# Kernel tuning notes

Measured on AMD Instinct MI355X. Metric: run time of the kernel, lower is better.

## Reference

```python
import jax, jax.numpy as jnp
import numpy as np
from jax import lax

NUM_STEPS = 100
T_FINAL = 1.0
BATCH = 16384
DIM = 64


def make_G(key, d, beta=1.0):
    # new_G: each G[:, :, k] is skew-symmetric, then globally rescaled so that
    # trace(L_G) == -0.5 * d, with L_G = 0.5 * einsum('ijk,jmk->im', G, G).
    F = jax.random.normal(key, (d, d, d), dtype=jnp.float32)  # F[:, :, k]
    G = 0.5 * (F - jnp.swapaxes(F, 0, 1))
    L_G = 0.5 * jnp.einsum('ijk,jmk->im', G, G)
    tr_L = jnp.trace(L_G)
    G = jnp.sqrt(-0.5 * d / tr_L) * G
    return jnp.sqrt(beta) * G


def setup_inputs() -> dict:
    key = jax.random.key(0)
    k_y0, k_t, k_G, k_dW = jax.random.split(key, 4)
    y0 = jax.random.normal(k_y0, (BATCH, DIM), dtype=jnp.float32)
    t = jax.random.uniform(k_t, (BATCH,), dtype=jnp.float32) * T_FINAL  # times in [0, T)
    G = make_G(k_G, DIM, beta=1.0)
    dt = T_FINAL / NUM_STEPS
    # Brownian increments for each RK4 step, dW ~ N(0, dt I)
    dW = jax.random.normal(k_dW, (NUM_STEPS, BATCH, DIM), dtype=jnp.float32) * np.sqrt(dt).astype(np.float32)
    return {"y0": y0, "t": t, "G": G, "dW": dW}


def reference(y0, t, G, dW):
    # multiplicativeNoise.sample -> sample_scheme: 100-step RK4 Stratonovich
    # integration of dY = mu_Strato dt + G(Y) o dB, then per-sample time gather.
    n = NUM_STEPS
    dt = T_FINAL / n
    L_G = 0.5 * jnp.einsum('ijk,jmk->im', G, G)  # [d, d]

    def mu_strato(y):
        # f(t,y) - 0.5 * div_Sigma(t,y) = L_G y - L_G y (kept explicit for faithfulness)
        f = jnp.einsum('ij,bj->bi', L_G, y)
        div_sigma = jnp.einsum('ij,bj->bi', 2.0 * L_G, y)
        return f - 0.5 * div_sigma

    def increment(y, dw):
        # drift * dt + (G y) . dW ; fuse the [b, d, d] diffusion contraction
        return mu_strato(y) * dt + jnp.einsum('ijk,bj,bk->bi', G, y, dw)

    def rk4_step(y, dw):
        k1 = increment(y, dw)
        k2 = increment(y + 0.5 * k1, dw)
        k3 = increment(y + 0.5 * k2, dw)
        k4 = increment(y + k3, dw)
        y_new = y + (k1 + 2.0 * k2 + 2.0 * k3 + k4) / 6.0
        return y_new, y_new

    _, ys = lax.scan(rk4_step, y0, dW)  # [n, b, d]

    # num_steps_int = trunc(n * t / T), clamped to n-1 when t >= T
    idx = jnp.clip(jnp.trunc(n * t / T_FINAL).astype(jnp.int32), 0, n - 1)  # [b]
    yt = ys[idx, jnp.arange(y0.shape[0])]  # [b, d]
    return yt
```

## Files before the change

### kernel.cpp

```cpp
#include <hip/hip_runtime.h>


typedef __attribute__((ext_vector_type(8))) short short8;
typedef __attribute__((ext_vector_type(4))) float f32x4;

#define NSTEP 100
#define BATCH 16384
#define NCHUNK 1024
#define ISTR 72
#define ESTR 4616

__device__ __forceinline__ unsigned short f2bf(float f) {
  unsigned u = __float_as_uint(f);
  unsigned r = (u + 0x7FFFu + ((u >> 16) & 1u)) >> 16;
  return (unsigned short)r;
}
__device__ __forceinline__ unsigned pack2(float a, float b) {
  return (unsigned)f2bf(a) | ((unsigned)f2bf(b) << 16);
}
__device__ __forceinline__ float bflo(unsigned u) { return __uint_as_float(u << 16); }
__device__ __forceinline__ float bfhi(unsigned u) { return __uint_as_float(u & 0xffff0000u); }


__global__ void k_swz(const float* __restrict__ G, unsigned short* __restrict__ g2s) {
  int o = blockIdx.x * blockDim.x + threadIdx.x;
  if (o < 64 * 64 * 64) {
    int nt = o >> 10;
    int r  = o & 1023;
    int l  = r >> 4;
    int c  = (r >> 3) & 1;
    int j  = r & 7;
    int n  = (nt << 4) + (l & 15);
    int k  = (c << 5) + ((l >> 4) << 3) + j;
    g2s[o] = f2bf(G[(n << 6) + k]);
  }
}

__global__ void k_idx(const float* __restrict__ t, int* __restrict__ idxb, int* __restrict__ hist) {
  int b = blockIdx.x * blockDim.x + threadIdx.x;
  if (b < BATCH) {
    int ix = (int)truncf(100.0f * t[b]);
    ix = min(max(ix, 0), NSTEP - 1);
    idxb[b] = ix;
    atomicAdd(&hist[ix], 1);
  }
}

__global__ void k_scan(const int* __restrict__ hist, int* __restrict__ offs) {
  if (threadIdx.x == 0 && blockIdx.x == 0) {
    int run = 0;
    for (int i = 0; i < NSTEP; ++i) { offs[i] = run; run += hist[i]; }
  }
}

__global__ void k_scatter(const int* __restrict__ idxb, const int* __restrict__ offs,
                          int* __restrict__ cur, int* __restrict__ perm) {
  int b = blockIdx.x * blockDim.x + threadIdx.x;
  if (b < BATCH) {
    int ix = idxb[b];
    int pos = offs[ix] + atomicAdd(&cur[ix], 1);
    perm[pos] = b;
  }
}


__device__ __forceinline__ float rk4_dot(const unsigned* Ap, const float* vr) {
  float a0 = 0.f, a1 = 0.f, a2 = 0.f, a3 = 0.f;
#pragma unroll
  for (int m = 0; m < 16; ++m) {
    float4 v = ((const float4*)vr)[m];
    unsigned ua = Ap[2 * m], ub = Ap[2 * m + 1];
    a0 = fmaf(bflo(ua), v.x, a0);
    a1 = fmaf(bfhi(ua), v.y, a1);
    a2 = fmaf(bflo(ub), v.z, a2);
    a3 = fmaf(bfhi(ub), v.w, a3);
  }
  return (a0 + a1) + (a2 + a3);
}

__device__ __forceinline__ float rk4_one(const unsigned short* Ar, float* vr, float y, int lane) {
  unsigned Areg[32];
#pragma unroll
  for (int m = 0; m < 8; ++m) {
    uint4 q = *(const uint4*)(Ar + (m << 3));
    Areg[4 * m + 0] = q.x; Areg[4 * m + 1] = q.y;
    Areg[4 * m + 2] = q.z; Areg[4 * m + 3] = q.w;
  }
  float k1 = rk4_dot(Areg, vr);
  vr[lane] = fmaf(0.5f, k1, y);
  float k2 = rk4_dot(Areg, vr);
  vr[lane] = fmaf(0.5f, k2, y);
  float k3 = rk4_dot(Areg, vr);
  vr[lane] = y + k3;
  float k4 = rk4_dot(Areg, vr);
  float yn = y + (k1 + 2.f * k2 + 2.f * k3 + k4) * (1.f / 6.f);
  vr[lane] = yn;
  return yn;
}

__global__ void __launch_bounds__(1024, 1) k_main(
    const float* __restrict__ y0, const float* __restrict__ dW,
    const unsigned short* __restrict__ G2S, const int* __restrict__ perm,
    const int* __restrict__ idxb, float* __restrict__ out)
{
  __shared__ __align__(16) unsigned short Abuf[16 * ESTR];
  __shared__ __align__(16) unsigned short dwst[1024];
  __shared__ __align__(16) float vbuf[16 * 64];
  __shared__ int meta_b[16], meta_i[16], chunk_max;

  const int t = threadIdx.x;
  const int lane = t & 63;
  const int wave = t >> 6;

  int W = blockIdx.x;
  int c = (W & 1) ? (NCHUNK - 1 - (W >> 1)) : (W >> 1);

  if (t < 16) {
    int b = perm[(c << 4) + t];
    meta_b[t] = b;
    meta_i[t] = idxb[b];
  }
  __syncthreads();
  if (t == 0) {
    int m = 0;
    for (int e = 0; e < 16; ++e) m = max(m, meta_i[e]);
    chunk_max = m;
  }
  const int my_b = meta_b[wave];
  const int my_idx = meta_i[wave];
  float y = y0[my_b * 64 + lane];
  vbuf[(wave << 6) + lane] = y;
  __syncthreads();
  const int nsteps = chunk_max + 1;

  const int fl = lane & 15;
  const int fq = lane >> 4;
  const int di = ((lane >> 3) << 7) + (wave << 3) + (lane & 7);
  float* vr = &vbuf[wave << 6];

  float dv = dW[(0 * BATCH + my_b) * 64 + lane];

  for (int s = 0; s < nsteps; ++s) {
    dwst[di] = f2bf(dv);
    if (s + 1 < nsteps) dv = dW[((s + 1) * BATCH + my_b) * 64 + lane];
    __syncthreads();

    {
      short8 a0 = *(const short8*)(&dwst[lane << 3]);
      short8 a1 = *(const short8*)(&dwst[512 + (lane << 3)]);
#pragma unroll 4
      for (int tt = 0; tt < 16; ++tt) {
        int nt = wave + (tt << 4);
        const unsigned short* gp = &G2S[(nt << 10) + (lane << 4)];
        short8 g0 = *(const short8*)(gp);
        short8 g1 = *(const short8*)(gp + 8);
        f32x4 acc = {0.f, 0.f, 0.f, 0.f};
        acc = __builtin_amdgcn_mfma_f32_16x16x32_bf16(g0, a0, acc, 0, 0, 0);
        acc = __builtin_amdgcn_mfma_f32_16x16x32_bf16(g1, a1, acc, 0, 0, 0);
        int i = nt >> 2;
        int j0 = ((nt & 3) << 4) + (fq << 2);
        uint2* dst = (uint2*)&Abuf[fl * ESTR + i * ISTR + j0];
        *dst = make_uint2(pack2(acc[0], acc[1]), pack2(acc[2], acc[3]));
      }
    }
    __syncthreads();

    {
      float yn = rk4_one(&Abuf[wave * ESTR + lane * ISTR], vr, y, lane);
      if (s == my_idx) out[my_b * 64 + lane] = yn;
      y = yn;
    }
  }
}


extern "C" void kernel_launch(void* const* d_in, const int* in_sizes, int n_in,
                              void* d_out, int out_size, void* d_ws, size_t ws_size,
                              hipStream_t stream) {
  const float* y0 = (const float*)d_in[0];
  const float* tv = (const float*)d_in[1];
  const float* G  = (const float*)d_in[2];
  const float* dW = (const float*)d_in[3];
  float* out = (float*)d_out;

  char* w = (char*)d_ws;
  unsigned short* g2s = (unsigned short*)w;
  int* idxb = (int*)(w + 524288);
  int* perm = (int*)(w + 524288 + 65536);
  int* hist = (int*)(w + 524288 + 131072);
  int* offs = hist + 128;
  int* cur  = hist + 256;

  hipMemsetAsync(hist, 0, 1536, stream);
  k_swz<<<1024, 256, 0, stream>>>(G, g2s);
  k_idx<<<64, 256, 0, stream>>>(tv, idxb, hist);
  k_scan<<<1, 64, 0, stream>>>(hist, offs);
  k_scatter<<<64, 256, 0, stream>>>(idxb, offs, cur, perm);
  k_main<<<NCHUNK, 1024, 0, stream>>>(y0, dW, g2s, perm, idxb, out);
}
```

Before: 2.623 ms.

## Run RK4 matvecs on MFMA with split-bf16 vectors and fuse prep kernels

The per-lane scalar FMA dot products in the four RK4 stages are replaced by MFMA bf16 instructions. Each wave's 64x64 A matrix is held in registers and the state vector is split into high and low bf16 parts to keep precision. The A matrix is written to shared memory in a swizzled, unpadded layout to avoid bank conflicts. The four preprocessing launches (swizzle, index, scan, scatter) and the memset are merged into one kernel, which cuts launch overhead. The cost is extra MFMA work on mostly wasted output lanes, lane-select logic, and a single-block serial histogram inside the prep kernel.

```diff
diff --git a/kernel.cpp b/kernel.cpp
--- a/kernel.cpp
+++ b/kernel.cpp
@@ -3,12 +3,11 @@
 
 typedef __attribute__((ext_vector_type(8))) short short8;
 typedef __attribute__((ext_vector_type(4))) float f32x4;
+typedef __attribute__((ext_vector_type(4))) unsigned u32x4;
 
 #define NSTEP 100
 #define BATCH 16384
 #define NCHUNK 1024
-#define ISTR 72
-#define ESTR 4616
 
 __device__ __forceinline__ unsigned short f2bf(float f) {
   unsigned u = __float_as_uint(f);
@@ -18,99 +17,90 @@
 __device__ __forceinline__ unsigned pack2(float a, float b) {
   return (unsigned)f2bf(a) | ((unsigned)f2bf(b) << 16);
 }
-__device__ __forceinline__ float bflo(unsigned u) { return __uint_as_float(u << 16); }
-__device__ __forceinline__ float bfhi(unsigned u) { return __uint_as_float(u & 0xffff0000u); }
-
-
-__global__ void k_swz(const float* __restrict__ G, unsigned short* __restrict__ g2s) {
-  int o = blockIdx.x * blockDim.x + threadIdx.x;
-  if (o < 64 * 64 * 64) {
+
+__device__ __forceinline__ short8 mk8(unsigned a, unsigned b, unsigned c, unsigned d) {
+  u32x4 u = {a, b, c, d};
+  return __builtin_bit_cast(short8, u);
+}
+
+__device__ __forceinline__ unsigned phi2(unsigned w0, unsigned w1) {
+  return (w0 >> 16) | (w1 & 0xffff0000u);
+}
+__device__ __forceinline__ unsigned plo2(unsigned w0, unsigned w1) {
+  return (w0 & 0xffffu) | (w1 << 16);
+}
+
+__device__ __forceinline__ float pick4(f32x4 a, bool b1, bool b2) {
+  float c0 = b2 ? a[2] : a[0];
+  float c1 = b2 ? a[3] : a[1];
+  return b1 ? c1 : c0;
+}
+
+__global__ void __launch_bounds__(256) k_prep(
+    const float* __restrict__ G, const float* __restrict__ tv,
+    unsigned short* __restrict__ g2s, int* __restrict__ idxb,
+    int* __restrict__ perm)
+{
+  if (blockIdx.x == 0) {
+    __shared__ int hist[NSTEP];
+    __shared__ int offs[NSTEP];
+    __shared__ int cur[NSTEP];
+    const int tid = threadIdx.x;
+    for (int i = tid; i < NSTEP; i += 256) { hist[i] = 0; cur[i] = 0; }
+    __syncthreads();
+    for (int r = 0; r < 64; ++r) {
+      int b = (r << 8) + tid;
+      int ix = (int)truncf(100.0f * tv[b]);
+      ix = min(max(ix, 0), NSTEP - 1);
+      idxb[b] = ix;
+      atomicAdd(&hist[ix], 1);
+    }
+    __syncthreads();
+    if (tid == 0) {
+      int run = 0;
+      for (int i = 0; i < NSTEP; ++i) { offs[i] = run; run += hist[i]; }
+    }
+    __syncthreads();
+    for (int r = 0; r < 64; ++r) {
+      int b = (r << 8) + tid;
+      int ix = idxb[b];
+      int pos = offs[ix] + atomicAdd(&cur[ix], 1);
+      perm[pos] = b;
+    }
+  } else {
+    int o  = ((blockIdx.x - 1) << 8) + threadIdx.x;
     int nt = o >> 10;
-    int r  = o & 1023;
-    int l  = r >> 4;
-    int c  = (r >> 3) & 1;
-    int j  = r & 7;
+    int r2 = o & 1023;
+    int l  = r2 >> 4;
+    int cc = (r2 >> 3) & 1;
+    int j  = r2 & 7;
     int n  = (nt << 4) + (l & 15);
-    int k  = (c << 5) + ((l >> 4) << 3) + j;
+    int k  = (cc << 5) + ((l >> 4) << 3) + j;
     g2s[o] = f2bf(G[(n << 6) + k]);
   }
 }
 
-__global__ void k_idx(const float* __restrict__ t, int* __restrict__ idxb, int* __restrict__ hist) {
-  int b = blockIdx.x * blockDim.x + threadIdx.x;
-  if (b < BATCH) {
-    int ix = (int)truncf(100.0f * t[b]);
-    ix = min(max(ix, 0), NSTEP - 1);
-    idxb[b] = ix;
-    atomicAdd(&hist[ix], 1);
-  }
-}
-
-__global__ void k_scan(const int* __restrict__ hist, int* __restrict__ offs) {
-  if (threadIdx.x == 0 && blockIdx.x == 0) {
-    int run = 0;
-    for (int i = 0; i < NSTEP; ++i) { offs[i] = run; run += hist[i]; }
-  }
-}
-
-__global__ void k_scatter(const int* __restrict__ idxb, const int* __restrict__ offs,
-                          int* __restrict__ cur, int* __restrict__ perm) {
-  int b = blockIdx.x * blockDim.x + threadIdx.x;
-  if (b < BATCH) {
-    int ix = idxb[b];
-    int pos = offs[ix] + atomicAdd(&cur[ix], 1);
-    perm[pos] = b;
-  }
-}
-
-
-__device__ __forceinline__ float rk4_dot(const unsigned* Ap, const float* vr) {
-  float a0 = 0.f, a1 = 0.f, a2 = 0.f, a3 = 0.f;
-#pragma unroll
-  for (int m = 0; m < 16; ++m) {
-    float4 v = ((const float4*)vr)[m];
-    unsigned ua = Ap[2 * m], ub = Ap[2 * m + 1];
-    a0 = fmaf(bflo(ua), v.x, a0);
-    a1 = fmaf(bfhi(ua), v.y, a1);
-    a2 = fmaf(bflo(ub), v.z, a2);
-    a3 = fmaf(bfhi(ub), v.w, a3);
-  }
-  return (a0 + a1) + (a2 + a3);
-}
-
-__device__ __forceinline__ float rk4_one(const unsigned short* Ar, float* vr, float y, int lane) {
-  unsigned Areg[32];
-#pragma unroll
-  for (int m = 0; m < 8; ++m) {
-    uint4 q = *(const uint4*)(Ar + (m << 3));
-    Areg[4 * m + 0] = q.x; Areg[4 * m + 1] = q.y;
-    Areg[4 * m + 2] = q.z; Areg[4 * m + 3] = q.w;
-  }
-  float k1 = rk4_dot(Areg, vr);
-  vr[lane] = fmaf(0.5f, k1, y);
-  float k2 = rk4_dot(Areg, vr);
-  vr[lane] = fmaf(0.5f, k2, y);
-  float k3 = rk4_dot(Areg, vr);
-  vr[lane] = y + k3;
-  float k4 = rk4_dot(Areg, vr);
-  float yn = y + (k1 + 2.f * k2 + 2.f * k3 + k4) * (1.f / 6.f);
-  vr[lane] = yn;
-  return yn;
-}
 
 __global__ void __launch_bounds__(1024, 1) k_main(
     const float* __restrict__ y0, const float* __restrict__ dW,
     const unsigned short* __restrict__ G2S, const int* __restrict__ perm,
     const int* __restrict__ idxb, float* __restrict__ out)
 {
-  __shared__ __align__(16) unsigned short Abuf[16 * ESTR];
+  __shared__ __align__(16) unsigned short Abuf[16 * 4096];
   __shared__ __align__(16) unsigned short dwst[1024];
-  __shared__ __align__(16) float vbuf[16 * 64];
+  __shared__ __align__(16) unsigned vbuf[16 * 64];
   __shared__ int meta_b[16], meta_i[16], chunk_max;
 
   const int t = threadIdx.x;
   const int lane = t & 63;
   const int wave = t >> 6;
+
+  {
+    u32x4 z = {0u, 0u, 0u, 0u};
+    u32x4* ab = (u32x4*)Abuf;
+#pragma unroll
+    for (int i = 0; i < 8; ++i) ab[t + (i << 10)] = z;
+  }
 
   int W = blockIdx.x;
   int c = (W & 1) ? (NCHUNK - 1 - (W >> 1)) : (W >> 1);
@@ -128,26 +118,48 @@
   }
   const int my_b = meta_b[wave];
   const int my_idx = meta_i[wave];
-  float y = y0[my_b * 64 + lane];
-  vbuf[(wave << 6) + lane] = y;
+
+  const int q = lane >> 4;
+  const int row = (((lane >> 2) & 3) << 4) | (q << 2) | (lane & 3);
+  const bool br1 = lane & 1, br2 = lane & 2, bt1 = lane & 4, bt2 = lane & 8;
+
+  unsigned* vb = &vbuf[wave << 6];
+  const uint4* vq0 = (const uint4*)(vb + (q << 3));
+  const uint4* vq1 = (const uint4*)(vb + 32 + (q << 3));
+
+  float y = y0[(my_b << 6) + row];
+  {
+    unsigned hb = (unsigned)f2bf(y);
+    float hif = __uint_as_float(hb << 16);
+    vb[row] = (hb << 16) | (unsigned)f2bf(y - hif);
+  }
   __syncthreads();
   const int nsteps = chunk_max + 1;
 
-  const int fl = lane & 15;
-  const int fq = lane >> 4;
   const int di = ((lane >> 3) << 7) + (wave << 3) + (lane & 7);
-  float* vr = &vbuf[wave << 6];
-
-  float dv = dW[(0 * BATCH + my_b) * 64 + lane];
+
+  const int ee = lane & 15;
+  const int qh = q & 1;
+  const int qv = q >> 1;
+  const int Gg = ((wave & 1) << 1) + qv;
+  const int wbase = (ee << 13) + (((wave & 3) >> 1) << 10) + (Gg << 8)
+                  + (((wave >> 2) & 3) << 4) + (qh << 3);
+  const int wx0 = ((ee & 7) ^ (Gg << 1)) << 4;
+
+  const unsigned swz_r = ((unsigned)((wave & 7) ^ ((lane >> 3) & 7))) << 4;
+  const char* abase = (const char*)Abuf + (wave << 13)
+                    + (((unsigned)(lane << 4)) ^ swz_r);
+
+  float dv = dW[(my_b << 6) + lane];
 
   for (int s = 0; s < nsteps; ++s) {
     dwst[di] = f2bf(dv);
-    if (s + 1 < nsteps) dv = dW[((s + 1) * BATCH + my_b) * 64 + lane];
+    if (s + 1 < nsteps) dv = dW[(((s + 1) * BATCH + my_b) << 6) + lane];
     __syncthreads();
 
     {
-      short8 a0 = *(const short8*)(&dwst[lane << 3]);
-      short8 a1 = *(const short8*)(&dwst[512 + (lane << 3)]);
+      short8 b0 = *(const short8*)(&dwst[lane << 3]);
+      short8 b1 = *(const short8*)(&dwst[512 + (lane << 3)]);
 #pragma unroll 4
       for (int tt = 0; tt < 16; ++tt) {
         int nt = wave + (tt << 4);
@@ -155,20 +167,77 @@
         short8 g0 = *(const short8*)(gp);
         short8 g1 = *(const short8*)(gp + 8);
         f32x4 acc = {0.f, 0.f, 0.f, 0.f};
-        acc = __builtin_amdgcn_mfma_f32_16x16x32_bf16(g0, a0, acc, 0, 0, 0);
-        acc = __builtin_amdgcn_mfma_f32_16x16x32_bf16(g1, a1, acc, 0, 0, 0);
-        int i = nt >> 2;
-        int j0 = ((nt & 3) << 4) + (fq << 2);
-        uint2* dst = (uint2*)&Abuf[fl * ESTR + i * ISTR + j0];
-        *dst = make_uint2(pack2(acc[0], acc[1]), pack2(acc[2], acc[3]));
+        acc = __builtin_amdgcn_mfma_f32_16x16x32_bf16(g0, b0, acc, 0, 0, 0);
+        acc = __builtin_amdgcn_mfma_f32_16x16x32_bf16(g1, b1, acc, 0, 0, 0);
+        int wbyte = (wbase + ((tt >> 2) << 11) + ((tt & 3) << 6))
+                  ^ (wx0 ^ (((tt & 3) >> 1) << 4));
+        *(uint2*)((char*)Abuf + wbyte) =
+            make_uint2(pack2(acc[0], acc[1]), pack2(acc[2], acc[3]));
       }
     }
     __syncthreads();
 
     {
-      float yn = rk4_one(&Abuf[wave * ESTR + lane * ISTR], vr, y, lane);
-      if (s == my_idx) out[my_b * 64 + lane] = yn;
+      short8 M00 = *(const short8*)(abase);
+      short8 M01 = *(const short8*)(abase + 1024);
+      short8 M10 = *(const short8*)(abase + 2048);
+      short8 M11 = *(const short8*)(abase + 3072);
+      short8 M20 = *(const short8*)(abase + 4096);
+      short8 M21 = *(const short8*)(abase + 5120);
+      short8 M30 = *(const short8*)(abase + 6144);
+      short8 M31 = *(const short8*)(abase + 7168);
+
+      auto stage_k = [&]() -> float {
+        uint4 A0 = vq0[0], A1 = vq0[1], B0 = vq1[0], B1 = vq1[1];
+        short8 h0 = mk8(phi2(A0.x, A0.y), phi2(A0.z, A0.w), phi2(A1.x, A1.y), phi2(A1.z, A1.w));
+        short8 l0 = mk8(plo2(A0.x, A0.y), plo2(A0.z, A0.w), plo2(A1.x, A1.y), plo2(A1.z, A1.w));
+        short8 h1 = mk8(phi2(B0.x, B0.y), phi2(B0.z, B0.w), phi2(B1.x, B1.y), phi2(B1.z, B1.w));
+        short8 l1 = mk8(plo2(B0.x, B0.y), plo2(B0.z, B0.w), plo2(B1.x, B1.y), plo2(B1.z, B1.w));
+        f32x4 a0 = {0.f, 0.f, 0.f, 0.f};
+        f32x4 a1 = a0, a2 = a0, a3 = a0;
+        a0 = __builtin_amdgcn_mfma_f32_16x16x32_bf16(M00, h0, a0, 0, 0, 0);
+        a1 = __builtin_amdgcn_mfma_f32_16x16x32_bf16(M10, h0, a1, 0, 0, 0);
+        a2 = __builtin_amdgcn_mfma_f32_16x16x32_bf16(M20, h0, a2, 0, 0, 0);
+        a3 = __builtin_amdgcn_mfma_f32_16x16x32_bf16(M30, h0, a3, 0, 0, 0);
+        a0 = __builtin_amdgcn_mfma_f32_16x16x32_bf16(M00, l0, a0, 0, 0, 0);
+        a1 = __builtin_amdgcn_mfma_f32_16x16x32_bf16(M10, l0, a1, 0, 0, 0);
+        a2 = __builtin_amdgcn_mfma_f32_16x16x32_bf16(M20, l0, a2, 0, 0, 0);
+        a3 = __builtin_amdgcn_mfma_f32_16x16x32_bf16(M30, l0, a3, 0, 0, 0);
+        a0 = __builtin_amdgcn_mfma_f32_16x16x32_bf16(M01, h1, a0, 0, 0, 0);
+        a1 = __builtin_amdgcn_mfma_f32_16x16x32_bf16(M11, h1, a1, 0, 0, 0);
+        a2 = __builtin_amdgcn_mfma_f32_16x16x32_bf16(M21, h1, a2, 0, 0, 0);
+        a3 = __builtin_amdgcn_mfma_f32_16x16x32_bf16(M31, h1, a3, 0, 0, 0);
+        a0 = __builtin_amdgcn_mfma_f32_16x16x32_bf16(M01, l1, a0, 0, 0, 0);
+        a1 = __builtin_amdgcn_mfma_f32_16x16x32_bf16(M11, l1, a1, 0, 0, 0);
+        a2 = __builtin_amdgcn_mfma_f32_16x16x32_bf16(M21, l1, a2, 0, 0, 0);
+        a3 = __builtin_amdgcn_mfma_f32_16x16x32_bf16(M31, l1, a3, 0, 0, 0);
+        float p0 = pick4(a0, br1, br2);
+        float p1 = pick4(a1, br1, br2);
+        float p2 = pick4(a2, br1, br2);
+        float p3 = pick4(a3, br1, br2);
+        float sl = bt1 ? p1 : p0;
+        float sh = bt1 ? p3 : p2;
+        return bt2 ? sh : sl;
+      };
+
+      auto wrv = [&](float v) {
+        unsigned hb = (unsigned)f2bf(v);
+        float hif = __uint_as_float(hb << 16);
+        vb[row] = (hb << 16) | (unsigned)f2bf(v - hif);
+        asm volatile("" ::: "memory");
+      };
+
+      float k1 = stage_k();
+      wrv(fmaf(0.5f, k1, y));
+      float k2 = stage_k();
+      wrv(fmaf(0.5f, k2, y));
+      float k3 = stage_k();
+      wrv(y + k3);
+      float k4 = stage_k();
+      float yn = fmaf(k1 + 2.f * k2 + 2.f * k3 + k4, (1.f / 6.f), y);
+      if (s == my_idx) out[(my_b << 6) + row] = yn;
       y = yn;
+      wrv(yn);
     }
   }
 }
@@ -187,14 +256,7 @@
   unsigned short* g2s = (unsigned short*)w;
   int* idxb = (int*)(w + 524288);
   int* perm = (int*)(w + 524288 + 65536);
-  int* hist = (int*)(w + 524288 + 131072);
-  int* offs = hist + 128;
-  int* cur  = hist + 256;
-
-  hipMemsetAsync(hist, 0, 1536, stream);
-  k_swz<<<1024, 256, 0, stream>>>(G, g2s);
-  k_idx<<<64, 256, 0, stream>>>(tv, idxb, hist);
-  k_scan<<<1, 64, 0, stream>>>(hist, offs);
-  k_scatter<<<64, 256, 0, stream>>>(idxb, offs, cur, perm);
+
+  k_prep<<<1025, 256, 0, stream>>>(G, tv, g2s, idxb, perm);
   k_main<<<NCHUNK, 1024, 0, stream>>>(y0, dW, g2s, perm, idxb, out);
 }
```

Measured after the change: 3.017 ms. 1.15x slower.
